# Performance work log

Hardware: AMD Instinct MI355X
Metric: run time of the kernel (lower is better)

The kernel has to match this reference:

```python
import jax, jax.numpy as jnp
import numpy as np

B, S, HID = 2, 2048, 1024
NH, NKV = 16, 4
HD = HID // NH          # 64
NREP = NH // NKV        # 4
EPS = 1e-06


def _rotate_half(x):
    h = x.shape[-1] // 2
    return jnp.concatenate([-x[..., h:], x[..., :h]], axis=-1)


def _rope(q, k, cos, sin):
    # q: [b,s,h,d], k: [b,s,kv,d]; cos/sin: [s,d] -> unsqueeze head dim
    c = cos[:, None, :]
    s = sin[:, None, :]
    return q * c + _rotate_half(q) * s, k * c + _rotate_half(k) * s


def setup_inputs() -> dict:
    key = jax.random.key(0)
    ks = jax.random.split(key, 8)
    sc = 0.02
    return {
        "x": jax.random.normal(ks[0], (B, S, HID), jnp.float32),
        "cos": jnp.cos(jnp.arange(S, dtype=jnp.float32)[:, None] *
                       (1.0 / (1e6 ** (jnp.arange(HD, dtype=jnp.float32) / HD)))),
        "sin": jnp.sin(jnp.arange(S, dtype=jnp.float32)[:, None] *
                       (1.0 / (1e6 ** (jnp.arange(HD, dtype=jnp.float32) / HD)))),
        "attention_mask": jnp.ones((B, S), jnp.int32),
        "Wq": jax.random.normal(ks[1], (HID, NH * HD), jnp.float32) * sc,
        "Wk": jax.random.normal(ks[2], (HID, NKV * HD), jnp.float32) * sc,
        "Wv": jax.random.normal(ks[3], (HID, NKV * HD), jnp.float32) * sc,
        "Wo": jax.random.normal(ks[4], (NH * HD, HID), jnp.float32) * sc,
    }


def reference(x, cos, sin, attention_mask, Wq, Wk, Wv, Wo):
    b, s, _ = x.shape
    q = (x @ Wq).reshape(b, s, NH, HD)
    k = (x @ Wk).reshape(b, s, NKV, HD)
    v = (x @ Wv).reshape(b, s, NKV, HD)
    q, k = _rope(q, k, cos[:s], sin[:s])
    # GQA repeat: [b,s,kv,d] -> [b,s,h,d]
    k = jnp.repeat(k, NREP, axis=2)
    v = jnp.repeat(v, NREP, axis=2)
    # -> [b,h,s,d]
    q = jnp.transpose(q, (0, 2, 1, 3))
    k = jnp.transpose(k, (0, 2, 1, 3))
    v = jnp.transpose(v, (0, 2, 1, 3))
    # feature map: elu(x) + 1 (positive features)
    q = jax.nn.elu(q) + 1.0
    k = jax.nn.elu(k) + 1.0
    # prefill path (seq_len > 1): non-causal kernelized scores
    scores = jnp.einsum("bhsd,bhtd->bhst", q, k)  # [b,h,s,s]
    mask = attention_mask[:, None, None, :]       # [b,1,1,s]
    scores = jnp.where(mask == 0, 0.0, scores)
    denom = jnp.clip(
        jax.lax.stop_gradient(jnp.abs(scores).sum(-1, keepdims=True)), 1e-06, None)
    scores = scores / denom
    out = jnp.einsum("bhst,bhtd->bhsd", scores, v)
    out = jnp.transpose(out, (0, 2, 1, 3)).reshape(b, s, NH * HD)
    return out @ Wo
```

## Files before the change

### kernel.cpp

```cpp
#include <hip/hip_runtime.h>
#include <hip/hip_bf16.h>

using u16 = unsigned short;
using u32 = unsigned int;

namespace {
constexpr int S   = 2048;
constexpr int HID = 1024;
constexpr int M   = 4096;
constexpr int K   = 1024;
}

typedef __attribute__((ext_vector_type(8))) short short8;
typedef __attribute__((ext_vector_type(4))) float f32x4;

__device__ __forceinline__ u16 f2bf(float f) {
    u32 u = __builtin_bit_cast(u32, f);
    u += 0x7fffu + ((u >> 16) & 1u);
    return (u16)(u >> 16);
}
__device__ __forceinline__ float bf2f(u16 h) {
    return __builtin_bit_cast(float, (u32)h << 16);
}
__device__ __forceinline__ float phi(float x) {
    return x > 0.f ? x + 1.f : __expf(x);
}
__device__ __forceinline__ void glds16(const u16* g, u16* l) {
    __builtin_amdgcn_global_load_lds(
        (const __attribute__((address_space(1))) u32*)g,
        (__attribute__((address_space(3))) u32*)l, 16, 0, 0);
}

template <int MODE>
__global__ __launch_bounds__(256, 3) void gemm_k(
    const u16* __restrict__ A, const u16* __restrict__ B,
    u16* __restrict__ Cq, float* __restrict__ Ckv,
    float* __restrict__ Cf, int ldc, int zAr, int zBr, int zCr,
    const float* __restrict__ Cos, const float* __restrict__ Sin,
    const int* __restrict__ Mask)
{
    constexpr int BK = 64;
    constexpr int NT = K / BK;
    __shared__ __align__(16) u16 sA0[64 * BK],  sA1[64 * BK];
    __shared__ __align__(16) u16 sB0[128 * BK], sB1[128 * BK];

    A += (size_t)blockIdx.z * zAr * K;
    B += (size_t)blockIdx.z * zBr * K;
    if (MODE == 1) Cf += (size_t)blockIdx.z * zCr * ldc;

    const int tid  = threadIdx.x;
    const int lane = tid & 63, w = tid >> 6;
    const int wm = w & 1, wn = w >> 1;
    const int m0 = blockIdx.x * 64, n0 = blockIdx.y * 128;
    const int fr = lane & 15, fq = lane >> 4;

    const int srow  = lane >> 3;
    const int sslot = lane & 7;
    const int sswz  = (sslot ^ srow) * 8;

    const u16* Asrc = A + (size_t)(m0 + w * 8 + srow) * K + sswz;
    const u16* Bsrc = B + (size_t)(n0 + w * 8 + srow) * K + sswz;
    const int ldsb = (w * 8) * BK;

    f32x4 acc[2][4] = {};

#define STAGE(dA, dB, kt)                                          \
    do {                                                           \
        glds16(Asrc + (kt),                 dA + ldsb);            \
        glds16(Asrc + (size_t)32 * K + (kt), dA + 32 * BK + ldsb); \
        glds16(Bsrc + (kt),                 dB + ldsb);            \
        glds16(Bsrc + (size_t)32 * K + (kt), dB + 32 * BK + ldsb); \
        glds16(Bsrc + (size_t)64 * K + (kt), dB + 64 * BK + ldsb); \
        glds16(Bsrc + (size_t)96 * K + (kt), dB + 96 * BK + ldsb); \
    } while (0)

#define COMPUTE(sAc, sBc)                                                    \
    do {                                                                     \
        _Pragma("unroll")                                                    \
        for (int kk = 0; kk < 2; ++kk) {                                     \
            const int ks = ((kk * 4 + fq) ^ (fr & 7)) * 8;                   \
            short8 ah[2], bh[4];                                             \
            _Pragma("unroll")                                                \
            for (int i = 0; i < 2; ++i)                                      \
                ah[i] = *(const short8*)(sAc + (wm * 32 + i * 16 + fr) * BK + ks); \
            _Pragma("unroll")                                                \
            for (int j = 0; j < 4; ++j)                                      \
                bh[j] = *(const short8*)(sBc + (wn * 64 + j * 16 + fr) * BK + ks); \
            _Pragma("unroll")                                                \
            for (int i = 0; i < 2; ++i)                                      \
                _Pragma("unroll")                                            \
                for (int j = 0; j < 4; ++j)                                  \
                    acc[i][j] = __builtin_amdgcn_mfma_f32_16x16x32_bf16(     \
                        ah[i], bh[j], acc[i][j], 0, 0, 0);                   \
        }                                                                    \
    } while (0)

    STAGE(sA0, sB0, 0);
    STAGE(sA1, sB1, BK);
#pragma unroll 1
    for (int t = 0; t < NT; t += 2) {
        asm volatile("s_waitcnt vmcnt(6)" ::: "memory");
        __builtin_amdgcn_s_barrier();
        COMPUTE(sA0, sB0);
        asm volatile("s_waitcnt lgkmcnt(0)" ::: "memory");
        __builtin_amdgcn_s_barrier();
        if (t + 2 < NT) STAGE(sA0, sB0, (t + 2) * BK);

        if (t + 2 < NT) asm volatile("s_waitcnt vmcnt(6)" ::: "memory");
        else            asm volatile("s_waitcnt vmcnt(0)" ::: "memory");
        __builtin_amdgcn_s_barrier();
        COMPUTE(sA1, sB1);
        asm volatile("s_waitcnt lgkmcnt(0)" ::: "memory");
        __builtin_amdgcn_s_barrier();
        if (t + 3 < NT) STAGE(sA1, sB1, (t + 3) * BK);
    }
#undef STAGE
#undef COMPUTE

    const bool isQ = (MODE == 0) && (n0 < 1024);
    const bool isK = (MODE == 0) && (n0 >= 1024) && (n0 < 1280);
#pragma unroll
    for (int i = 0; i < 2; ++i)
#pragma unroll
        for (int jj = 0; jj < 4; ++jj) {
            const int row = m0 + wm * 32 + i * 16 + fq * 4 + jj;
            float v0 = acc[i][0][jj], v1 = acc[i][1][jj];
            float v2 = acc[i][2][jj], v3 = acc[i][3][jj];
            if (MODE == 1) {
                float* cr = &Cf[(size_t)row * ldc + n0 + wn * 64 + fr];
                cr[0] = v0; cr[16] = v1; cr[32] = v2; cr[48] = v3;
                continue;
            }
            if (isQ || isK) {
                const int sb = (row & (S - 1)) * 64;
                float r0 = v0 * Cos[sb + fr]      - v2 * Sin[sb + fr];
                float r2 = v2 * Cos[sb + fr + 32] + v0 * Sin[sb + fr + 32];
                float r1 = v1 * Cos[sb + fr + 16] - v3 * Sin[sb + fr + 16];
                float r3 = v3 * Cos[sb + fr + 48] + v1 * Sin[sb + fr + 48];
                v0 = phi(r0); v1 = phi(r1); v2 = phi(r2); v3 = phi(r3);
            }
            if (isQ) {
                u16* cr = &Cq[(size_t)row * 1024 + n0 + wn * 64 + fr];
                cr[0]  = f2bf(v0); cr[16] = f2bf(v1);
                cr[32] = f2bf(v2); cr[48] = f2bf(v3);
            } else if (isK) {
                const float mv = (float)Mask[row];
                float* cr = &Ckv[(size_t)row * 512 + (n0 - 1024) + wn * 64 + fr];
                cr[0] = v0 * mv; cr[16] = v1 * mv;
                cr[32] = v2 * mv; cr[48] = v3 * mv;
            } else {
                float* cr = &Ckv[(size_t)row * 512 + 256 + (n0 - 1280) + wn * 64 + fr];
                cr[0] = v0; cr[16] = v1; cr[32] = v2; cr[48] = v3;
            }
        }
}

__global__ __launch_bounds__(256) void prep_k(
    const float* __restrict__ X,  u16* __restrict__ Xb,
    const float* __restrict__ Wq, const float* __restrict__ Wk,
    const float* __restrict__ Wv, const float* __restrict__ Wo,
    u16* __restrict__ wt, u16* __restrict__ wot)
{
    const int bid = blockIdx.x, tid = threadIdx.x;
    if (bid < 4096) {
        const int i = (bid * 256 + tid) * 4;
        float4 v = *reinterpret_cast<const float4*>(&X[i]);
        ushort4 h;
        h.x = f2bf(v.x); h.y = f2bf(v.y); h.z = f2bf(v.z); h.w = f2bf(v.w);
        *reinterpret_cast<ushort4*>(&Xb[i]) = h;
        return;
    }
    int r = bid - 4096;
    const float* W; u16* T; int N, nbase, bx, by;
    if (r < 1024)      { W = Wq; T = wt;  N = 1024; nbase = 0;    bx = r & 31; by = r >> 5; }
    else if (r < 1280) { r -= 1024; W = Wk; T = wt; N = 256; nbase = 1024; bx = r & 7; by = r >> 3; }
    else if (r < 1536) { r -= 1280; W = Wv; T = wt; N = 256; nbase = 1280; bx = r & 7; by = r >> 3; }
    else               { r -= 1536; W = Wo; T = wot; N = 1024; nbase = 0;  bx = r & 31; by = r >> 5; }

    __shared__ float t[32][33];
    const int n0 = bx * 32, k0 = by * 32;
    const int tx = tid & 31, ty = tid >> 5;
#pragma unroll
    for (int i = 0; i < 4; ++i)
        t[ty + i * 8][tx] = W[(size_t)(k0 + ty + i * 8) * N + n0 + tx];
    __syncthreads();
#pragma unroll
    for (int i = 0; i < 4; ++i) {
        const int n = ty + i * 8;
        T[(size_t)(nbase + n0 + n) * 1024 + k0 + tx] = f2bf(t[tx][n]);
    }
}

__global__ __launch_bounds__(256) void kv_stage1_k(
    const float* __restrict__ KVf, float* __restrict__ part)
{
    const int g  = blockIdx.x;
    const int ch = blockIdx.y;
    const int b  = g >> 2, kvh = g & 3;
    const int tid = threadIdx.x;

    __shared__ float ks[64][64];
    __shared__ float vs[64][64];
    const int m0 = b * S + ch * 64;
#pragma unroll
    for (int l = 0; l < 4; ++l) {
        int idx = tid + l * 256;
        int r = idx >> 4, q4 = (idx & 15) * 4;
        const float* src = KVf + (size_t)(m0 + r) * 512 + kvh * 64;
        *reinterpret_cast<float4*>(&ks[r][q4]) = *reinterpret_cast<const float4*>(src + q4);
        *reinterpret_cast<float4*>(&vs[r][q4]) = *reinterpret_cast<const float4*>(src + 256 + q4);
    }
    __syncthreads();

    const int i = tid >> 2, j0 = (tid & 3) * 16;
    float4 a0 = {0,0,0,0}, a1 = {0,0,0,0}, a2 = {0,0,0,0}, a3 = {0,0,0,0};
#pragma unroll 8
    for (int r = 0; r < 64; ++r) {
        float kv = ks[r][i];
        float4 w0 = *reinterpret_cast<const float4*>(&vs[r][j0]);
        float4 w1 = *reinterpret_cast<const float4*>(&vs[r][j0 + 4]);
        float4 w2 = *reinterpret_cast<const float4*>(&vs[r][j0 + 8]);
        float4 w3 = *reinterpret_cast<const float4*>(&vs[r][j0 + 12]);
        a0.x = fmaf(kv, w0.x, a0.x); a0.y = fmaf(kv, w0.y, a0.y);
        a0.z = fmaf(kv, w0.z, a0.z); a0.w = fmaf(kv, w0.w, a0.w);
        a1.x = fmaf(kv, w1.x, a1.x); a1.y = fmaf(kv, w1.y, a1.y);
        a1.z = fmaf(kv, w1.z, a1.z); a1.w = fmaf(kv, w1.w, a1.w);
        a2.x = fmaf(kv, w2.x, a2.x); a2.y = fmaf(kv, w2.y, a2.y);
        a2.z = fmaf(kv, w2.z, a2.z); a2.w = fmaf(kv, w2.w, a2.w);
        a3.x = fmaf(kv, w3.x, a3.x); a3.y = fmaf(kv, w3.y, a3.y);
        a3.z = fmaf(kv, w3.z, a3.z); a3.w = fmaf(kv, w3.w, a3.w);
    }
    float* dst = part + ((size_t)g * 32 + ch) * 4160;
    float* d0 = dst + i * 64 + j0;
    *reinterpret_cast<float4*>(d0)      = a0;
    *reinterpret_cast<float4*>(d0 + 4)  = a1;
    *reinterpret_cast<float4*>(d0 + 8)  = a2;
    *reinterpret_cast<float4*>(d0 + 12) = a3;
    if (tid < 64) {
        float ksum = 0.f;
#pragma unroll 8
        for (int r = 0; r < 64; ++r) ksum += ks[r][tid];
        dst[4096 + tid] = ksum;
    }
}

__global__ __launch_bounds__(256) void kv_reduce_k(
    const float* __restrict__ part, u16* __restrict__ KVh,
    float* __restrict__ Ksumf)
{
    const int g = blockIdx.x;
    const int e = blockIdx.y * 256 + threadIdx.x;
    if (e >= 4160) return;
    const float* p = part + (size_t)g * 32 * 4160 + e;
    float s = 0.f;
#pragma unroll 8
    for (int c = 0; c < 32; ++c) s += p[(size_t)c * 4160];
    if (e < 4096) KVh[g * 4096 + e] = f2bf(s);
    else          Ksumf[g * 64 + (e - 4096)] = s;
}

__global__ __launch_bounds__(256) void kwqhat_k(
    const u16* __restrict__ WoT, const u16* __restrict__ KVb,
    u16* __restrict__ KWT,
    const u16* __restrict__ Qt, const float* __restrict__ Ksumf,
    u16* __restrict__ Qh)
{
    const int tid = threadIdx.x;
    if (blockIdx.x >= 256) {
        const int t = (blockIdx.x - 256) * 256 + tid;
        const int m = t >> 4, h = t & 15;
        const int g = (m >> 11) * 4 + (h >> 2);
        const u16* q  = Qt + (size_t)m * 1024 + h * 64;
        const float* Ks = Ksumf + g * 64;

        float qv[64];
        float den = 0.f;
#pragma unroll
        for (int c = 0; c < 8; ++c) {
            short8 v8 = *reinterpret_cast<const short8*>(q + c * 8);
#pragma unroll
            for (int j = 0; j < 8; ++j) {
                qv[c * 8 + j] = bf2f((u16)v8[j]);
                den = fmaf(qv[c * 8 + j], Ks[c * 8 + j], den);
            }
        }
        const float rd = 1.f / fmaxf(den, 1e-6f);
        u16* o = Qh + (size_t)m * 1024 + h * 64;
#pragma unroll
        for (int c = 0; c < 8; ++c) {
            short8 ov;
#pragma unroll
            for (int j = 0; j < 8; ++j) ov[j] = (short)f2bf(qv[c * 8 + j] * rd);
            *reinterpret_cast<short8*>(o + c * 8) = ov;
        }
        return;
    }
    __shared__ __align__(16) u16 sA[128 * 64];
    __shared__ __align__(16) u16 sB[64 * 64];

    const int lane = tid & 63, w = tid >> 6;
    const int o0 = (blockIdx.x & 7) * 128;
    const int gh = blockIdx.x >> 3, b = gh >> 4, h = gh & 15, g = b * 4 + (h >> 2);
    const int fr = lane & 15, fq = lane >> 4;
    const int srow = lane >> 3, sslot = lane & 7;
    const int sswz = (sslot ^ srow) * 8;

#pragma unroll
    for (int c = 0; c < 4; ++c) {
        const int rb = w * 32 + c * 8;
        glds16(WoT + (size_t)(o0 + rb + srow) * 1024 + h * 64 + sswz, sA + rb * 64);
    }
#pragma unroll
    for (int c = 0; c < 2; ++c) {
        const int rb = w * 16 + c * 8;
        glds16(KVb + (size_t)g * 4096 + (rb + srow) * 64 + sswz, sB + rb * 64);
    }
    asm volatile("s_waitcnt vmcnt(0)" ::: "memory");
    __syncthreads();

    f32x4 acc[2][4] = {};
#pragma unroll
    for (int kk = 0; kk < 2; ++kk) {
        short8 a_h[2], b_h[4];
#pragma unroll
        for (int i = 0; i < 2; ++i) {
            const int row = w * 32 + i * 16 + fr;
            a_h[i] = *(const short8*)(sA + row * 64 + ((kk * 4 + fq) ^ (fr & 7)) * 8);
        }
#pragma unroll
        for (int j = 0; j < 4; ++j) {
            const int row = j * 16 + fr;
            b_h[j] = *(const short8*)(sB + row * 64 + ((kk * 4 + fq) ^ (fr & 7)) * 8);
        }
#pragma unroll
        for (int i = 0; i < 2; ++i)
#pragma unroll
            for (int j = 0; j < 4; ++j)
                acc[i][j] = __builtin_amdgcn_mfma_f32_16x16x32_bf16(
                    a_h[i], b_h[j], acc[i][j], 0, 0, 0);
    }
#pragma unroll
    for (int i = 0; i < 2; ++i)
#pragma unroll
        for (int j = 0; j < 4; ++j)
#pragma unroll
            for (int jj = 0; jj < 4; ++jj) {
                const int row = o0 + w * 32 + i * 16 + fq * 4 + jj;
                const int col = j * 16 + fr;
                KWT[((size_t)b * 1024 + row) * 1024 + h * 64 + col] =
                    f2bf(acc[i][j][jj]);
            }
}

extern "C" void kernel_launch(void* const* d_in, const int* in_sizes, int n_in,
                              void* d_out, int out_size, void* d_ws, size_t ws_size,
                              hipStream_t stream)
{
    const float* x    = (const float*)d_in[0];
    const float* cosp = (const float*)d_in[1];
    const float* sinp = (const float*)d_in[2];
    const int*   msk  = (const int*)d_in[3];
    const float* Wq   = (const float*)d_in[4];
    const float* Wk   = (const float*)d_in[5];
    const float* Wv   = (const float*)d_in[6];
    const float* Wo   = (const float*)d_in[7];
    float* out = (float*)d_out;

    u16* xbf  = (u16*)d_ws;
    u16* wt   = xbf  + (size_t)M * K;
    u16* wot  = wt   + (size_t)1536 * K;
    u16* qt   = wot  + (size_t)K * K;
    u16* qhat = qt   + (size_t)M * K;
    u16* kvb  = qhat + (size_t)M * K;
    u16* kwt  = kvb  + 8 * 4096;
    float* kvf   = (float*)(kwt + (size_t)2 * K * K);
    float* part  = kvf + (size_t)M * 512;
    float* ksumf = part + (size_t)8 * 32 * 4160;

    prep_k<<<4096 + 1024 + 256 + 256 + 1024, 256, 0, stream>>>(
        x, xbf, Wq, Wk, Wv, Wo, wt, wot);

    gemm_k<0><<<dim3(M / 64, 1536 / 128, 1), 256, 0, stream>>>(
        xbf, wt, qt, kvf, nullptr, 0, 0, 0, 0, cosp, sinp, msk);

    kv_stage1_k<<<dim3(8, 32), 256, 0, stream>>>(kvf, part);
    kv_reduce_k<<<dim3(8, 17), 256, 0, stream>>>(part, kvb, ksumf);

    kwqhat_k<<<512, 256, 0, stream>>>(wot, kvb, kwt, qt, ksumf, qhat);

    gemm_k<1><<<dim3(2048 / 64, HID / 128, 2), 256, 0, stream>>>(
        qhat, kwt, nullptr, nullptr, out, HID, 2048, 1024, 2048,
        nullptr, nullptr, nullptr);
}
```

Measured before the change: 70.22 us.

## Fuse x bf16 conversion and Q normalization into GEMM A-tile loads

The first GEMM now reads x in fp32 straight from global memory and converts it to bf16 in registers before writing the LDS tile. This removes the separate conversion pass in prep_k and the bf16 copy of x it wrote. The output GEMM reads unnormalized Q plus a per-row, per-head reciprocal denominator and scales Q while staging, so the materialized qhat buffer is gone. In exchange the A path switches from async global-to-LDS loads to register loads followed by VALU conversion and LDS stores, which adds extra waits and register pressure inside the pipelined loop.

```diff
diff --git a/kernel.cpp b/kernel.cpp
--- a/kernel.cpp
+++ b/kernel.cpp
@@ -30,10 +30,25 @@
         (const __attribute__((address_space(1))) u32*)g,
         (__attribute__((address_space(3))) u32*)l, 16, 0, 0);
 }
+__device__ __forceinline__ short8 cvt8(float4 lo, float4 hi) {
+    short8 s;
+    s[0] = (short)f2bf(lo.x); s[1] = (short)f2bf(lo.y);
+    s[2] = (short)f2bf(lo.z); s[3] = (short)f2bf(lo.w);
+    s[4] = (short)f2bf(hi.x); s[5] = (short)f2bf(hi.y);
+    s[6] = (short)f2bf(hi.z); s[7] = (short)f2bf(hi.w);
+    return s;
+}
+__device__ __forceinline__ short8 scale8(short8 q, float r) {
+    short8 s;
+#pragma unroll
+    for (int j = 0; j < 8; ++j) s[j] = (short)f2bf(bf2f((u16)q[j]) * r);
+    return s;
+}
 
 template <int MODE>
 __global__ __launch_bounds__(256, 3) void gemm_k(
-    const u16* __restrict__ A, const u16* __restrict__ B,
+    const float* __restrict__ Af, const u16* __restrict__ Ab,
+    const float* __restrict__ Rden, const u16* __restrict__ B,
     u16* __restrict__ Cq, float* __restrict__ Ckv,
     float* __restrict__ Cf, int ldc, int zAr, int zBr, int zCr,
     const float* __restrict__ Cos, const float* __restrict__ Sin,
@@ -44,9 +59,12 @@
     __shared__ __align__(16) u16 sA0[64 * BK],  sA1[64 * BK];
     __shared__ __align__(16) u16 sB0[128 * BK], sB1[128 * BK];
 
-    A += (size_t)blockIdx.z * zAr * K;
+    if (MODE == 1) {
+        Ab   += (size_t)blockIdx.z * zAr * K;
+        Rden += (size_t)blockIdx.z * zAr * 16;
+        Cf   += (size_t)blockIdx.z * zCr * ldc;
+    }
     B += (size_t)blockIdx.z * zBr * K;
-    if (MODE == 1) Cf += (size_t)blockIdx.z * zCr * ldc;
 
     const int tid  = threadIdx.x;
     const int lane = tid & 63, w = tid >> 6;
@@ -56,22 +74,53 @@
 
     const int srow  = lane >> 3;
     const int sslot = lane & 7;
-    const int sswz  = (sslot ^ srow) * 8;
-
-    const u16* Asrc = A + (size_t)(m0 + w * 8 + srow) * K + sswz;
-    const u16* Bsrc = B + (size_t)(n0 + w * 8 + srow) * K + sswz;
+    const int aswz  = (sslot ^ srow) * 8;
+
+    const int arow0 = m0 + w * 8 + srow;
+    const int arow1 = arow0 + 32;
+    const u16* Bsrc = B + (size_t)(n0 + w * 8 + srow) * K + aswz;
     const int ldsb = (w * 8) * BK;
+    u16* const wa0 = (u16*)0 + (w * 8 + srow) * BK + sslot * 8;
+    const int aoff0 = (w * 8 + srow) * BK + sslot * 8;
+    const int aoff1 = (w * 8 + 32 + srow) * BK + sslot * 8;
+    (void)wa0;
 
     f32x4 acc[2][4] = {};
 
-#define STAGE(dA, dB, kt)                                          \
+    float4 xa0, xb0, xc0, xd0, xa1, xb1, xc1, xd1;
+    short8 qa0, qb0, qa1, qb1;
+    float  ra0, rb0, ra1, rb1;
+
+#define STAGE_B(dB, kt)                                            \
     do {                                                           \
-        glds16(Asrc + (kt),                 dA + ldsb);            \
-        glds16(Asrc + (size_t)32 * K + (kt), dA + 32 * BK + ldsb); \
-        glds16(Bsrc + (kt),                 dB + ldsb);            \
+        glds16(Bsrc + (kt),                  dB + ldsb);           \
         glds16(Bsrc + (size_t)32 * K + (kt), dB + 32 * BK + ldsb); \
         glds16(Bsrc + (size_t)64 * K + (kt), dB + 64 * BK + ldsb); \
         glds16(Bsrc + (size_t)96 * K + (kt), dB + 96 * BK + ldsb); \
+    } while (0)
+
+#define LOAD_A(X, kt)                                                        \
+    do {                                                                     \
+        if (MODE == 0) {                                                     \
+            xa##X = *(const float4*)&Af[(size_t)arow0 * 1024 + (kt) + aswz]; \
+            xb##X = *(const float4*)&Af[(size_t)arow0 * 1024 + (kt) + aswz + 4]; \
+            xc##X = *(const float4*)&Af[(size_t)arow1 * 1024 + (kt) + aswz]; \
+            xd##X = *(const float4*)&Af[(size_t)arow1 * 1024 + (kt) + aswz + 4]; \
+        } else {                                                             \
+            qa##X = *(const short8*)&Ab[(size_t)arow0 * 1024 + (kt) + aswz]; \
+            qb##X = *(const short8*)&Ab[(size_t)arow1 * 1024 + (kt) + aswz]; \
+            ra##X = Rden[arow0 * 16 + ((kt) >> 6)];                          \
+            rb##X = Rden[arow1 * 16 + ((kt) >> 6)];                          \
+        }                                                                    \
+    } while (0)
+
+#define WRITE_A(X, sAc)                                                      \
+    do {                                                                     \
+        short8 s0_, s1_;                                                     \
+        if (MODE == 0) { s0_ = cvt8(xa##X, xb##X); s1_ = cvt8(xc##X, xd##X); } \
+        else           { s0_ = scale8(qa##X, ra##X); s1_ = scale8(qb##X, rb##X); } \
+        *(short8*)(sAc + aoff0) = s0_;                                       \
+        *(short8*)(sAc + aoff1) = s1_;                                       \
     } while (0)
 
 #define COMPUTE(sAc, sBc)                                                    \
@@ -95,26 +144,32 @@
         }                                                                    \
     } while (0)
 
-    STAGE(sA0, sB0, 0);
-    STAGE(sA1, sB1, BK);
+    STAGE_B(sB0, 0);  LOAD_A(0, 0);
+    STAGE_B(sB1, BK); LOAD_A(1, BK);
 #pragma unroll 1
     for (int t = 0; t < NT; t += 2) {
-        asm volatile("s_waitcnt vmcnt(6)" ::: "memory");
+        asm volatile("s_waitcnt vmcnt(8)" ::: "memory");
+        WRITE_A(0, sA0);
+        asm volatile("s_waitcnt lgkmcnt(0)" ::: "memory");
         __builtin_amdgcn_s_barrier();
         COMPUTE(sA0, sB0);
         asm volatile("s_waitcnt lgkmcnt(0)" ::: "memory");
         __builtin_amdgcn_s_barrier();
-        if (t + 2 < NT) STAGE(sA0, sB0, (t + 2) * BK);
-
-        if (t + 2 < NT) asm volatile("s_waitcnt vmcnt(6)" ::: "memory");
+        if (t + 2 < NT) { STAGE_B(sB0, (t + 2) * BK); LOAD_A(0, (t + 2) * BK); }
+
+        if (t + 2 < NT) asm volatile("s_waitcnt vmcnt(8)" ::: "memory");
         else            asm volatile("s_waitcnt vmcnt(0)" ::: "memory");
+        WRITE_A(1, sA1);
+        asm volatile("s_waitcnt lgkmcnt(0)" ::: "memory");
         __builtin_amdgcn_s_barrier();
         COMPUTE(sA1, sB1);
         asm volatile("s_waitcnt lgkmcnt(0)" ::: "memory");
         __builtin_amdgcn_s_barrier();
-        if (t + 3 < NT) STAGE(sA1, sB1, (t + 3) * BK);
-    }
-#undef STAGE
+        if (t + 3 < NT) { STAGE_B(sB1, (t + 3) * BK); LOAD_A(1, (t + 3) * BK); }
+    }
+#undef STAGE_B
+#undef LOAD_A
+#undef WRITE_A
 #undef COMPUTE
 
     const bool isQ = (MODE == 0) && (n0 < 1024);
@@ -156,21 +211,12 @@
 }
 
 __global__ __launch_bounds__(256) void prep_k(
-    const float* __restrict__ X,  u16* __restrict__ Xb,
     const float* __restrict__ Wq, const float* __restrict__ Wk,
     const float* __restrict__ Wv, const float* __restrict__ Wo,
     u16* __restrict__ wt, u16* __restrict__ wot)
 {
-    const int bid = blockIdx.x, tid = threadIdx.x;
-    if (bid < 4096) {
-        const int i = (bid * 256 + tid) * 4;
-        float4 v = *reinterpret_cast<const float4*>(&X[i]);
-        ushort4 h;
-        h.x = f2bf(v.x); h.y = f2bf(v.y); h.z = f2bf(v.z); h.w = f2bf(v.w);
-        *reinterpret_cast<ushort4*>(&Xb[i]) = h;
-        return;
-    }
-    int r = bid - 4096;
+    int r = blockIdx.x;
+    const int tid = threadIdx.x;
     const float* W; u16* T; int N, nbase, bx, by;
     if (r < 1024)      { W = Wq; T = wt;  N = 1024; nbase = 0;    bx = r & 31; by = r >> 5; }
     else if (r < 1280) { r -= 1024; W = Wk; T = wt; N = 256; nbase = 1024; bx = r & 7; by = r >> 3; }
@@ -259,11 +305,11 @@
     else          Ksumf[g * 64 + (e - 4096)] = s;
 }
 
-__global__ __launch_bounds__(256) void kwqhat_k(
+__global__ __launch_bounds__(256) void kwden_k(
     const u16* __restrict__ WoT, const u16* __restrict__ KVb,
     u16* __restrict__ KWT,
     const u16* __restrict__ Qt, const float* __restrict__ Ksumf,
-    u16* __restrict__ Qh)
+    float* __restrict__ Rden)
 {
     const int tid = threadIdx.x;
     if (blockIdx.x >= 256) {
@@ -273,26 +319,15 @@
         const u16* q  = Qt + (size_t)m * 1024 + h * 64;
         const float* Ks = Ksumf + g * 64;
 
-        float qv[64];
         float den = 0.f;
 #pragma unroll
         for (int c = 0; c < 8; ++c) {
             short8 v8 = *reinterpret_cast<const short8*>(q + c * 8);
 #pragma unroll
-            for (int j = 0; j < 8; ++j) {
-                qv[c * 8 + j] = bf2f((u16)v8[j]);
-                den = fmaf(qv[c * 8 + j], Ks[c * 8 + j], den);
-            }
+            for (int j = 0; j < 8; ++j)
+                den = fmaf(bf2f((u16)v8[j]), Ks[c * 8 + j], den);
         }
-        const float rd = 1.f / fmaxf(den, 1e-6f);
-        u16* o = Qh + (size_t)m * 1024 + h * 64;
-#pragma unroll
-        for (int c = 0; c < 8; ++c) {
-            short8 ov;
-#pragma unroll
-            for (int j = 0; j < 8; ++j) ov[j] = (short)f2bf(qv[c * 8 + j] * rd);
-            *reinterpret_cast<short8*>(o + c * 8) = ov;
-        }
+        Rden[m * 16 + h] = 1.f / fmaxf(den, 1e-6f);
         return;
     }
     __shared__ __align__(16) u16 sA[128 * 64];
@@ -366,29 +401,29 @@
     const float* Wo   = (const float*)d_in[7];
     float* out = (float*)d_out;
 
-    u16* xbf  = (u16*)d_ws;
-    u16* wt   = xbf  + (size_t)M * K;
+    u16* wt   = (u16*)d_ws;
     u16* wot  = wt   + (size_t)1536 * K;
     u16* qt   = wot  + (size_t)K * K;
-    u16* qhat = qt   + (size_t)M * K;
-    u16* kvb  = qhat + (size_t)M * K;
+    u16* kvb  = qt   + (size_t)M * K;
     u16* kwt  = kvb  + 8 * 4096;
     float* kvf   = (float*)(kwt + (size_t)2 * K * K);
     float* part  = kvf + (size_t)M * 512;
     float* ksumf = part + (size_t)8 * 32 * 4160;
-
-    prep_k<<<4096 + 1024 + 256 + 256 + 1024, 256, 0, stream>>>(
-        x, xbf, Wq, Wk, Wv, Wo, wt, wot);
+    float* rden  = ksumf + 512;
+
+    prep_k<<<1024 + 256 + 256 + 1024, 256, 0, stream>>>(
+        Wq, Wk, Wv, Wo, wt, wot);
 
     gemm_k<0><<<dim3(M / 64, 1536 / 128, 1), 256, 0, stream>>>(
-        xbf, wt, qt, kvf, nullptr, 0, 0, 0, 0, cosp, sinp, msk);
+        x, nullptr, nullptr, wt, qt, kvf, nullptr, 0, 0, 0, 0,
+        cosp, sinp, msk);
 
     kv_stage1_k<<<dim3(8, 32), 256, 0, stream>>>(kvf, part);
     kv_reduce_k<<<dim3(8, 17), 256, 0, stream>>>(part, kvb, ksumf);
 
-    kwqhat_k<<<512, 256, 0, stream>>>(wot, kvb, kwt, qt, ksumf, qhat);
+    kwden_k<<<512, 256, 0, stream>>>(wot, kvb, kwt, qt, ksumf, rden);
 
     gemm_k<1><<<dim3(2048 / 64, HID / 128, 2), 256, 0, stream>>>(
-        qhat, kwt, nullptr, nullptr, out, HID, 2048, 1024, 2048,
+        nullptr, qt, rden, kwt, nullptr, nullptr, out, HID, 2048, 1024, 2048,
         nullptr, nullptr, nullptr);
 }
```

New measurement: 71.13 us. No clear change (+1.3%).

## Store K/V projections as bf16 and fuse KV reduction into stage1 via atomic counter

Applied to the files above, without the earlier changes.

K and V projection outputs are now written as bf16 instead of fp32, halving that intermediate's write and read traffic. The separate kv_reduce kernel is removed. The last-arriving stage1 block for each group, found with an atomic counter that prep_k zeroes, now does the 32-chunk reduction itself with float4 loads. This saves one kernel launch and some memory traffic, but adds bf16 rounding of K and V before the KV product and leaves a single block per group doing a serial tail reduction.

```diff
diff --git a/kernel.cpp b/kernel.cpp
--- a/kernel.cpp
+++ b/kernel.cpp
@@ -34,7 +34,7 @@
 template <int MODE>
 __global__ __launch_bounds__(256, 3) void gemm_k(
     const u16* __restrict__ A, const u16* __restrict__ B,
-    u16* __restrict__ Cq, float* __restrict__ Ckv,
+    u16* __restrict__ Cq, u16* __restrict__ Ckv,
     float* __restrict__ Cf, int ldc, int zAr, int zBr, int zCr,
     const float* __restrict__ Cos, const float* __restrict__ Sin,
     const int* __restrict__ Mask)
@@ -145,12 +145,13 @@
                 cr[32] = f2bf(v2); cr[48] = f2bf(v3);
             } else if (isK) {
                 const float mv = (float)Mask[row];
-                float* cr = &Ckv[(size_t)row * 512 + (n0 - 1024) + wn * 64 + fr];
-                cr[0] = v0 * mv; cr[16] = v1 * mv;
-                cr[32] = v2 * mv; cr[48] = v3 * mv;
+                u16* cr = &Ckv[(size_t)row * 512 + (n0 - 1024) + wn * 64 + fr];
+                cr[0]  = f2bf(v0 * mv); cr[16] = f2bf(v1 * mv);
+                cr[32] = f2bf(v2 * mv); cr[48] = f2bf(v3 * mv);
             } else {
-                float* cr = &Ckv[(size_t)row * 512 + 256 + (n0 - 1280) + wn * 64 + fr];
-                cr[0] = v0; cr[16] = v1; cr[32] = v2; cr[48] = v3;
+                u16* cr = &Ckv[(size_t)row * 512 + 256 + (n0 - 1280) + wn * 64 + fr];
+                cr[0]  = f2bf(v0); cr[16] = f2bf(v1);
+                cr[32] = f2bf(v2); cr[48] = f2bf(v3);
             }
         }
 }
@@ -159,9 +160,10 @@
     const float* __restrict__ X,  u16* __restrict__ Xb,
     const float* __restrict__ Wq, const float* __restrict__ Wk,
     const float* __restrict__ Wv, const float* __restrict__ Wo,
-    u16* __restrict__ wt, u16* __restrict__ wot)
+    u16* __restrict__ wt, u16* __restrict__ wot, int* __restrict__ cnt)
 {
     const int bid = blockIdx.x, tid = threadIdx.x;
+    if (bid == 0 && tid < 8) cnt[tid] = 0;
     if (bid < 4096) {
         const int i = (bid * 256 + tid) * 4;
         float4 v = *reinterpret_cast<const float4*>(&X[i]);
@@ -192,7 +194,8 @@
 }
 
 __global__ __launch_bounds__(256) void kv_stage1_k(
-    const float* __restrict__ KVf, float* __restrict__ part)
+    const u16* __restrict__ KVf, float* __restrict__ part,
+    u16* __restrict__ KVh, float* __restrict__ Ksumf, int* __restrict__ cnt)
 {
     const int g  = blockIdx.x;
     const int ch = blockIdx.y;
@@ -201,14 +204,20 @@
 
     __shared__ float ks[64][64];
     __shared__ float vs[64][64];
+    __shared__ int isred;
     const int m0 = b * S + ch * 64;
 #pragma unroll
-    for (int l = 0; l < 4; ++l) {
+    for (int l = 0; l < 2; ++l) {
         int idx = tid + l * 256;
-        int r = idx >> 4, q4 = (idx & 15) * 4;
-        const float* src = KVf + (size_t)(m0 + r) * 512 + kvh * 64;
-        *reinterpret_cast<float4*>(&ks[r][q4]) = *reinterpret_cast<const float4*>(src + q4);
-        *reinterpret_cast<float4*>(&vs[r][q4]) = *reinterpret_cast<const float4*>(src + 256 + q4);
+        int r = idx >> 3, c8 = (idx & 7) * 8;
+        const u16* src = KVf + (size_t)(m0 + r) * 512 + kvh * 64 + c8;
+        short8 k8 = *reinterpret_cast<const short8*>(src);
+        short8 v8 = *reinterpret_cast<const short8*>(src + 256);
+#pragma unroll
+        for (int j = 0; j < 8; ++j) {
+            ks[r][c8 + j] = bf2f((u16)k8[j]);
+            vs[r][c8 + j] = bf2f((u16)v8[j]);
+        }
     }
     __syncthreads();
 
@@ -242,21 +251,34 @@
         for (int r = 0; r < 64; ++r) ksum += ks[r][tid];
         dst[4096 + tid] = ksum;
     }
-}
-
-__global__ __launch_bounds__(256) void kv_reduce_k(
-    const float* __restrict__ part, u16* __restrict__ KVh,
-    float* __restrict__ Ksumf)
-{
-    const int g = blockIdx.x;
-    const int e = blockIdx.y * 256 + threadIdx.x;
-    if (e >= 4160) return;
-    const float* p = part + (size_t)g * 32 * 4160 + e;
-    float s = 0.f;
-#pragma unroll 8
-    for (int c = 0; c < 32; ++c) s += p[(size_t)c * 4160];
-    if (e < 4096) KVh[g * 4096 + e] = f2bf(s);
-    else          Ksumf[g * 64 + (e - 4096)] = s;
+
+    __syncthreads();
+    if (tid == 0) {
+        __threadfence();
+        int old = atomicAdd(&cnt[g], 1);
+        isred = (old == 31);
+        if (isred) __threadfence();
+    }
+    __syncthreads();
+    if (!isred) return;
+
+    const float* p = part + (size_t)g * 32 * 4160;
+#pragma unroll 1
+    for (int e4 = tid; e4 < 1040; e4 += 256) {
+        float4 s = {0.f, 0.f, 0.f, 0.f};
+#pragma unroll
+        for (int c = 0; c < 32; ++c) {
+            float4 v = *reinterpret_cast<const float4*>(&p[(size_t)c * 4160 + e4 * 4]);
+            s.x += v.x; s.y += v.y; s.z += v.z; s.w += v.w;
+        }
+        if (e4 < 1024) {
+            ushort4 h;
+            h.x = f2bf(s.x); h.y = f2bf(s.y); h.z = f2bf(s.z); h.w = f2bf(s.w);
+            *reinterpret_cast<ushort4*>(&KVh[g * 4096 + e4 * 4]) = h;
+        } else {
+            *reinterpret_cast<float4*>(&Ksumf[g * 64 + (e4 - 1024) * 4]) = s;
+        }
+    }
 }
 
 __global__ __launch_bounds__(256) void kwqhat_k(
@@ -373,18 +395,18 @@
     u16* qhat = qt   + (size_t)M * K;
     u16* kvb  = qhat + (size_t)M * K;
     u16* kwt  = kvb  + 8 * 4096;
-    float* kvf   = (float*)(kwt + (size_t)2 * K * K);
-    float* part  = kvf + (size_t)M * 512;
+    u16* kvfb = kwt  + (size_t)2 * K * K;
+    float* part  = (float*)(kvfb + (size_t)M * 512);
     float* ksumf = part + (size_t)8 * 32 * 4160;
+    int*   cnt   = (int*)(ksumf + 512);
 
     prep_k<<<4096 + 1024 + 256 + 256 + 1024, 256, 0, stream>>>(
-        x, xbf, Wq, Wk, Wv, Wo, wt, wot);
+        x, xbf, Wq, Wk, Wv, Wo, wt, wot, cnt);
 
     gemm_k<0><<<dim3(M / 64, 1536 / 128, 1), 256, 0, stream>>>(
-        xbf, wt, qt, kvf, nullptr, 0, 0, 0, 0, cosp, sinp, msk);
-
-    kv_stage1_k<<<dim3(8, 32), 256, 0, stream>>>(kvf, part);
-    kv_reduce_k<<<dim3(8, 17), 256, 0, stream>>>(part, kvb, ksumf);
+        xbf, wt, qt, kvfb, nullptr, 0, 0, 0, 0, cosp, sinp, msk);
+
+    kv_stage1_k<<<dim3(8, 32), 256, 0, stream>>>(kvfb, part, kvb, ksumf, cnt);
 
     kwqhat_k<<<512, 256, 0, stream>>>(wot, kvb, kwt, qt, ksumf, qhat);
 
```

After: 83.56 us. 19.0% more time.
